# Optimization experiments

Measured on AMD Instinct MI355X. Metric: run time of the kernel, lower is better.

The kernel has to match this reference:

```python
import jax, jax.numpy as jnp
import numpy as np

NEG_INF = -9e15  # matches torch code's -9000000000000000.0
ALPHA = 0.1      # LeakyReLU negative slope


def setup_inputs() -> dict:
    key = jax.random.key(0)
    k1, k2, k3, k4 = jax.random.split(key, 4)
    N, D = 4096, 2048
    input_features = jax.random.normal(k1, (N, D), dtype=jnp.float32)
    adj_mat = jax.random.normal(k2, (N, N), dtype=jnp.float32)
    # parameters of GraphAttentionLayer(2048, 2048)
    W = jax.random.normal(k3, (D, D), dtype=jnp.float32) * 0.02
    a = jax.random.normal(k4, (2 * D, 1), dtype=jnp.float32) * 0.02
    return {"input_features": input_features, "adj_mat": adj_mat, "W": W, "a": a}


def reference(input_features, adj_mat, W, a):
    x = input_features  # [N, D]
    D = W.shape[1]
    # --- GNN.forward: cosine similarity adjacency ---
    dot = x @ x.T                                  # [N, N]
    lens = jnp.sqrt(jnp.sum(x * x, axis=1))        # [N]
    cos_sim = dot / (lens[:, None] * lens[None, :])
    new_adj = adj_mat * cos_sim                    # [N, N]
    # --- GraphAttentionLayer.forward ---
    h = x @ W                                      # [N, D]
    # concat trick: e_ij = leakyrelu(a1.h_i + a2.h_j), avoiding O(N^2*2D) tensor
    a1, a2 = a[:D, 0], a[D:, 0]
    s1 = h @ a1                                    # [N]
    s2 = h @ a2                                    # [N]
    e = jax.nn.leaky_relu(s1[:, None] + s2[None, :], ALPHA)  # [N, N]
    att_logits = jnp.where(new_adj > 0, e, NEG_INF)
    attention = jax.nn.softmax(att_logits, axis=1)  # dropout is identity at eval
    h_prime = attention @ h                        # [N, D]
    return jax.nn.elu(h_prime)                     # concat=True -> elu
```

## Files before the change

### kernel.cpp

```cpp
#include <hip/hip_runtime.h>
#include <hip/hip_bf16.h>
#include <cmath>

typedef unsigned short u16;
typedef unsigned char u8;
typedef unsigned int u32;
typedef __attribute__((ext_vector_type(8))) _Float16 f16x8;
typedef __attribute__((ext_vector_type(4))) float f32x4;

__device__ __forceinline__ float bf2f(u16 v) {
    union { u32 u; float f; } c; c.u = (u32)v << 16; return c.f;
}
__device__ __forceinline__ u16 f2bf(float f) {
    union { float f; u32 u; } c; c.f = f;
    u32 u = c.u;
    u += 0x7FFF + ((u >> 16) & 1);
    return (u16)(u >> 16);
}
__device__ __forceinline__ u16 f2h(float f) {
    _Float16 h = (_Float16)f; u16 r; __builtin_memcpy(&r, &h, 2); return r;
}
__device__ __forceinline__ float h2f(u16 b) {
    _Float16 h; __builtin_memcpy(&h, &b, 2); return (float)h;
}

__device__ __forceinline__ void gld_lds16(const void* g, void* l) {
    __builtin_amdgcn_global_load_lds(
        (const __attribute__((address_space(1))) void*)g,
        (__attribute__((address_space(3))) void*)l, 16, 0, 0);
}

__global__ __launch_bounds__(256) void sniff_kernel(const u16* __restrict__ x,
                                                    u32* __restrict__ flag) {
    const int t = threadIdx.x;
    int local = 0;
    for (int i = t; i < 4096; i += 256) {
        const int e = (x[i] >> 7) & 0xFF;
        if (e >= 110 && e <= 137) local++;
    }
#pragma unroll
    for (int o = 32; o > 0; o >>= 1) local += __shfl_down(local, o, 64);
    __shared__ int s[4];
    if ((t & 63) == 0) s[t >> 6] = local;
    __syncthreads();
    if (t == 0) {
        const int tot = s[0] + s[1] + s[2] + s[3];
        *flag = (tot >= 3200) ? 1u : 0u;
    }
}

__global__ __launch_bounds__(256) void prep_kernel(
    const void* __restrict__ xin, const void* __restrict__ Win,
    const void* __restrict__ ain,
    u16* __restrict__ xhi, u16* __restrict__ xlo,
    u16* __restrict__ WT, u16* __restrict__ aout,
    const u32* __restrict__ flag, int N, int D)
{
    __shared__ u16 tile[64][68];
    const bool isbf = (*flag != 0);
    const int b = blockIdx.x;
    const int t = threadIdx.x;

    if (b < 1024) {
        const long base = (long)b * 8192;
#pragma unroll
        for (int it = 0; it < 8; ++it) {
            const long i = base + (long)(it * 256 + t) * 4;
            float v[4];
            if (isbf) {
                ushort4 u = *(const ushort4*)((const u16*)xin + i);
                v[0] = bf2f(u.x); v[1] = bf2f(u.y); v[2] = bf2f(u.z); v[3] = bf2f(u.w);
            } else {
                float4 f = *(const float4*)((const float*)xin + i);
                v[0] = f.x; v[1] = f.y; v[2] = f.z; v[3] = f.w;
            }
            ushort4 hi, lo;
            u16* hp = &hi.x; u16* lp = &lo.x;
#pragma unroll
            for (int k = 0; k < 4; ++k) {
                _Float16 h = (_Float16)v[k];
                u16 hb; __builtin_memcpy(&hb, &h, 2);
                hp[k] = hb;
                lp[k] = f2h(v[k] - (float)h);
            }
            *(ushort4*)(xhi + i) = hi;
            *(ushort4*)(xlo + i) = lo;
        }
    } else if (b < 2048) {
        const int tt = b - 1024;
        const int bc = (tt & 31) * 64;
        const int br = (tt >> 5) * 64;
        const int lr = t >> 4;
        const int lc = (t & 15) * 4;
#pragma unroll
        for (int s = 0; s < 4; ++s) {
            const int r = lr + s * 16;
            float v[4];
            if (isbf) {
                ushort4 u = *(const ushort4*)((const u16*)Win + (size_t)(br + r) * D + bc + lc);
                v[0] = bf2f(u.x); v[1] = bf2f(u.y); v[2] = bf2f(u.z); v[3] = bf2f(u.w);
            } else {
                float4 f = *(const float4*)((const float*)Win + (size_t)(br + r) * D + bc + lc);
                v[0] = f.x; v[1] = f.y; v[2] = f.z; v[3] = f.w;
            }
            tile[r][lc + 0] = f2h(v[0]); tile[r][lc + 1] = f2h(v[1]);
            tile[r][lc + 2] = f2h(v[2]); tile[r][lc + 3] = f2h(v[3]);
        }
        __syncthreads();
#pragma unroll
        for (int s = 0; s < 4; ++s) {
            const int oc = lr + s * 16;
            ushort4 v;
            v.x = tile[lc + 0][oc]; v.y = tile[lc + 1][oc];
            v.z = tile[lc + 2][oc]; v.w = tile[lc + 3][oc];
            *(ushort4*)&WT[(size_t)(bc + oc) * D + br + lc] = v;
        }
    } else {
        for (int i = t; i < 2 * D; i += 256) {
            float v = isbf ? bf2f(((const u16*)ain)[i]) : ((const float*)ain)[i];
            aout[i] = f2h(v);
        }
    }
}

#define NMASK 528
#define MAXFIX 1024
__global__ __launch_bounds__(256, 2) void fused_mask_h(
    const u16* __restrict__ Xhi, const u16* __restrict__ Xlo, int ldx,
    u16* __restrict__ P, int N,
    const void* __restrict__ adj,
    const u16* __restrict__ WT, int D,
    u16* __restrict__ h,
    const u32* __restrict__ dflag)
{
    __shared__ alignas(16) u8 smem[32768];

    const int tid = threadIdx.x;
    const int wave = tid >> 6, lane = tid & 63;
    const int wr = wave >> 1, wc = wave & 1;
    const int srow = lane >> 2, slot = lane & 3;
    const int q = lane >> 4, mrow = lane & 15;

    if (blockIdx.x < NMASK) {
        const int idx = blockIdx.x;
        int bm = (int)((__builtin_sqrtf(8.0f * idx + 1.0f) - 1.0f) * 0.5f);
        while ((bm + 1) * (bm + 2) / 2 <= idx) ++bm;
        while (bm * (bm + 1) / 2 > idx) --bm;
        const int bn = idx - bm * (bm + 1) / 2;

        u16* smAh = (u16*)smem;
        u16* smBh = (u16*)(smem + 8192);

        const u16* Ah = Xhi + (size_t)bm * 128 * ldx;
        const u16* Bh = Xhi + (size_t)bn * 128 * ldx;

        f32x4 acc[4][4] = {};

        for (int kt = 0; kt < ldx; kt += 32) {
#pragma unroll
            for (int r = 0; r < 2; ++r) {
                const int rb = r * 64 + wave * 16;
                const size_t goff = (size_t)(rb + srow) * ldx + kt + slot * 8;
                gld_lds16(Ah + goff, &smAh[rb * 32]);
                gld_lds16(Bh + goff, &smBh[rb * 32]);
            }
            __syncthreads();

            f16x8 ah[4], bh[4];
#pragma unroll
            for (int i = 0; i < 4; ++i) {
                ah[i] = *(const f16x8*)&smAh[(wr * 64 + i * 16 + mrow) * 32 + q * 8];
                bh[i] = *(const f16x8*)&smBh[(wc * 64 + i * 16 + mrow) * 32 + q * 8];
            }
#pragma unroll
            for (int i = 0; i < 4; ++i)
#pragma unroll
                for (int j = 0; j < 4; ++j)
                    acc[i][j] = __builtin_amdgcn_mfma_f32_16x16x32_f16(
                        ah[i], bh[j], acc[i][j], 0, 0, 0);
            __syncthreads();
        }

        const bool isbf = (*dflag != 0);
        const u16* adjB = (const u16*)adj;
        const float* adjF = (const float*)adj;

        u8* sgn = smem;
        u32* list = (u32*)(smem + 24576);
        int* cntp = (int*)(smem + 28672);

        if (tid == 0) *cntp = 0;
        const float tau = isbf ? -1.0f : 0.125f;

#pragma unroll
        for (int i = 0; i < 4; ++i)
#pragma unroll
            for (int j = 0; j < 4; ++j)
#pragma unroll
                for (int r = 0; r < 4; ++r) {
                    const int rl = wr * 64 + i * 16 + q * 4 + r;
                    const int cl = wc * 64 + j * 16 + mrow;
                    const float v = acc[i][j][r];
                    sgn[rl * 132 + cl] = v > 0.f ? (u8)1
                                       : (v < 0.f ? (u8)2 : (u8)0);
                }
        __syncthreads();

#pragma unroll
        for (int i = 0; i < 4; ++i)
#pragma unroll
            for (int j = 0; j < 4; ++j)
#pragma unroll
                for (int r = 0; r < 4; ++r) {
                    const float v = acc[i][j][r];
                    if (__builtin_fabsf(v) < tau) {
                        const int rl = wr * 64 + i * 16 + q * 4 + r;
                        const int cl = wc * 64 + j * 16 + mrow;
                        const int ix = atomicAdd(cntp, 1);
                        if (ix < MAXFIX) list[ix] = (u32)((rl << 8) | cl);
                    }
                }
        __syncthreads();

        const int nfix = (*cntp < MAXFIX) ? *cntp : MAXFIX;
        for (int e = wave; e < nfix; e += 4) {
            const u32 pk = list[e];
            const int rl = (int)(pk >> 8), cl = (int)(pk & 255u);
            const u16* arh = Xhi + (size_t)(bm * 128 + rl) * ldx;
            const u16* arl = Xlo + (size_t)(bm * 128 + rl) * ldx;
            const u16* brh = Xhi + (size_t)(bn * 128 + cl) * ldx;
            const u16* brl = Xlo + (size_t)(bn * 128 + cl) * ldx;
            float ssum = 0.f;
#pragma unroll
            for (int kk = 0; kk < 4; ++kk) {
                const int k = kk * 512 + lane * 8;
                const f16x8 vah = *(const f16x8*)&arh[k];
                const f16x8 val2 = *(const f16x8*)&arl[k];
                const f16x8 vbh = *(const f16x8*)&brh[k];
                const f16x8 vbl = *(const f16x8*)&brl[k];
#pragma unroll
                for (int u = 0; u < 8; ++u)
                    ssum += ((float)vah[u] + (float)val2[u]) *
                            ((float)vbh[u] + (float)vbl[u]);
            }
#pragma unroll
            for (int o = 32; o > 0; o >>= 1) ssum += __shfl_xor(ssum, o, 64);
            if (lane == 0)
                sgn[rl * 132 + cl] = ssum > 0.f ? (u8)1
                                   : (ssum < 0.f ? (u8)2 : (u8)0);
        }
        __syncthreads();

        {
            const int c = tid & 127;
            const int r0 = tid >> 7;
#pragma unroll 4
            for (int s = 0; s < 64; ++s) {
                const int rr = r0 + 2 * s;
                const u8 s3 = sgn[rr * 132 + c];
                const size_t aidx = (size_t)(bm * 128 + rr) * N + bn * 128 + c;
                const float av = isbf ? bf2f(adjB[aidx]) : adjF[aidx];
                const bool f = (s3 == 1) ? (av > 0.f)
                             : (s3 == 2) ? (av < 0.f) : false;
                P[aidx] = f ? (u16)1 : (u16)0;
            }
        }

        if (bm != bn) {
            const int bl_ = tid & 63;
            const int a0 = tid >> 6;
#pragma unroll 4
            for (int s = 0; s < 32; ++s) {
                const int a = a0 + 4 * s;
#pragma unroll
                for (int hb = 0; hb < 2; ++hb) {
                    const int b = bl_ + 64 * hb;
                    const u8 s3 = sgn[b * 132 + a];
                    const size_t aidx = (size_t)(bn * 128 + a) * N + bm * 128 + b;
                    const float av = isbf ? bf2f(adjB[aidx]) : adjF[aidx];
                    const bool f = (s3 == 1) ? (av > 0.f)
                                 : (s3 == 2) ? (av < 0.f) : false;
                    P[aidx] = f ? (u16)1 : (u16)0;
                }
            }
        }
    } else {
        const int j = blockIdx.x - NMASK;
        const int bn = j & 15;
        const int bm = j >> 4;

        u16* smA = (u16*)smem;
        u16* smB = (u16*)(smem + 8192);

        const u16* Ab = Xhi + (size_t)bm * 128 * ldx;
        const u16* Bb = WT + (size_t)bn * 128 * D;

        f32x4 acc[4][4] = {};

        for (int kt = 0; kt < D; kt += 32) {
#pragma unroll
            for (int r = 0; r < 2; ++r) {
                const int rb = r * 64 + wave * 16;
                const int gr = rb + srow;
                gld_lds16(Ab + (size_t)gr * ldx + kt + slot * 8, &smA[rb * 32]);
                gld_lds16(Bb + (size_t)gr * D + kt + slot * 8, &smB[rb * 32]);
            }
            __syncthreads();

            f16x8 af[4], bfr[4];
#pragma unroll
            for (int i = 0; i < 4; ++i) {
                af[i]  = *(const f16x8*)&smA[(wr * 64 + i * 16 + mrow) * 32 + q * 8];
                bfr[i] = *(const f16x8*)&smB[(wc * 64 + i * 16 + mrow) * 32 + q * 8];
            }
#pragma unroll
            for (int i = 0; i < 4; ++i)
#pragma unroll
                for (int jj = 0; jj < 4; ++jj)
                    acc[i][jj] = __builtin_amdgcn_mfma_f32_16x16x32_f16(
                        af[i], bfr[jj], acc[i][jj], 0, 0, 0);
            __syncthreads();
        }

        const int col0 = bn * 128 + wc * 64 + mrow;
        const int row0 = bm * 128 + wr * 64 + q * 4;
#pragma unroll
        for (int i = 0; i < 4; ++i)
#pragma unroll
            for (int jj = 0; jj < 4; ++jj)
#pragma unroll
                for (int r = 0; r < 4; ++r)
                    h[(size_t)(row0 + i * 16 + r) * D + col0 + jj * 16] =
                        f2h(acc[i][jj][r]);
    }
}

__global__ __launch_bounds__(256) void post1_kernel(
    const u16* __restrict__ h, const u16* __restrict__ a,
    float* __restrict__ s1, float* __restrict__ s2,
    u16* __restrict__ hT, int N, int D)
{
    __shared__ u16 tile[64][68];
    __shared__ float r1[4], r2[4];
    const int b = blockIdx.x;
    const int t = threadIdx.x;

    if (b < N) {
        const u16* hr = h + (size_t)b * D;
        const int k0 = t * 8;
        float acc1 = 0.f, acc2 = 0.f;
#pragma unroll
        for (int u = 0; u < 8; u += 4) {
            ushort4 hv  = *(const ushort4*)&hr[k0 + u];
            ushort4 a1v = *(const ushort4*)&a[k0 + u];
            ushort4 a2v = *(const ushort4*)&a[D + k0 + u];
            acc1 += h2f(hv.x) * h2f(a1v.x) + h2f(hv.y) * h2f(a1v.y)
                  + h2f(hv.z) * h2f(a1v.z) + h2f(hv.w) * h2f(a1v.w);
            acc2 += h2f(hv.x) * h2f(a2v.x) + h2f(hv.y) * h2f(a2v.y)
                  + h2f(hv.z) * h2f(a2v.z) + h2f(hv.w) * h2f(a2v.w);
        }
        const int lane = t & 63, wv = t >> 6;
#pragma unroll
        for (int o = 32; o > 0; o >>= 1) {
            acc1 += __shfl_down(acc1, o, 64);
            acc2 += __shfl_down(acc2, o, 64);
        }
        if (lane == 0) { r1[wv] = acc1; r2[wv] = acc2; }
        __syncthreads();
        if (t == 0) {
            s1[b] = r1[0] + r1[1] + r1[2] + r1[3];
            s2[b] = r2[0] + r2[1] + r2[2] + r2[3];
        }
    } else {
        const int tt = b - N;
        const int bc = (tt & 31) * 64;
        const int br = (tt >> 5) * 64;
        const int lr = t >> 4;
        const int lc = (t & 15) * 4;
#pragma unroll
        for (int s = 0; s < 4; ++s) {
            const int r = lr + s * 16;
            ushort4 v = *(const ushort4*)&h[(size_t)(br + r) * D + bc + lc];
            tile[r][lc + 0] = v.x; tile[r][lc + 1] = v.y;
            tile[r][lc + 2] = v.z; tile[r][lc + 3] = v.w;
        }
        __syncthreads();
#pragma unroll
        for (int s = 0; s < 4; ++s) {
            const int oc = lr + s * 16;
            ushort4 v;
            v.x = tile[lc + 0][oc]; v.y = tile[lc + 1][oc];
            v.z = tile[lc + 2][oc]; v.w = tile[lc + 3][oc];
            *(ushort4*)&hT[(size_t)(bc + oc) * N + br + lc] = v;
        }
    }
}

__global__ __launch_bounds__(256) void softmax_kernel(
    u16* __restrict__ P, const float* __restrict__ s1,
    const float* __restrict__ s2, int N)
{
    const int row = blockIdx.x;
    const int t = threadIdx.x;
    const int lane = t & 63, wv = t >> 6;
    u16* prow = P + (size_t)row * N;
    const float s1v = s1[row];

    float e[16];
#pragma unroll
    for (int it = 0; it < 16; ++it) {
        const int j = it * 256 + t;
        const u16 f = prow[j];
        float ev = s1v + s2[j];
        ev = ev >= 0.f ? ev : 0.1f * ev;
        e[it] = f ? ev : -9.0e15f;
    }
    float m = -3.4e38f;
#pragma unroll
    for (int it = 0; it < 16; ++it) m = fmaxf(m, e[it]);
#pragma unroll
    for (int o = 32; o > 0; o >>= 1) m = fmaxf(m, __shfl_xor(m, o, 64));
    __shared__ float red[8];
    if (lane == 0) red[wv] = m;
    __syncthreads();
    m = fmaxf(fmaxf(red[0], red[1]), fmaxf(red[2], red[3]));

    float sum = 0.f;
#pragma unroll
    for (int it = 0; it < 16; ++it) {
        e[it] = expf(fminf(e[it] - m, 0.0f));
        sum += e[it];
    }
#pragma unroll
    for (int o = 32; o > 0; o >>= 1) sum += __shfl_xor(sum, o, 64);
    if (lane == 0) red[4 + wv] = sum;
    __syncthreads();
    sum = red[4] + red[5] + red[6] + red[7];
    const float inv = 1.f / fmaxf(sum, 1e-30f);
#pragma unroll
    for (int it = 0; it < 16; ++it) {
        const int j = it * 256 + t;
        prow[j] = f2h(e[it] * inv);
    }
}

__global__ __launch_bounds__(256, 2) void gemm_elu(
    const u16* __restrict__ A, int lda,
    const u16* __restrict__ B, int ldb,
    u16* __restrict__ C, int ldc,
    int K, const u32* __restrict__ dflag)
{
    __shared__ alignas(16) u16 smA[64 * 32];
    __shared__ alignas(16) u16 smB[128 * 32];

    const int tid = threadIdx.x;
    const int wave = tid >> 6, lane = tid & 63;
    const int bm = blockIdx.y, bn = blockIdx.x;

    const u16* Ab = A + (size_t)bm * 64 * lda;
    const u16* Bb = B + (size_t)bn * 128 * ldb;

    const int srow = lane >> 2, slot = lane & 3;
    const int q = lane >> 4, mrow = lane & 15;

    f32x4 acc[4][2] = {};

    for (int kt = 0; kt < K; kt += 32) {
        {
            const int rb = wave * 16;
            gld_lds16(Ab + (size_t)(rb + srow) * lda + kt + slot * 8, &smA[rb * 32]);
        }
#pragma unroll
        for (int r = 0; r < 2; ++r) {
            const int rb = r * 64 + wave * 16;
            gld_lds16(Bb + (size_t)(rb + srow) * ldb + kt + slot * 8, &smB[rb * 32]);
        }
        __syncthreads();

        f16x8 af[4], bfr[2];
#pragma unroll
        for (int i = 0; i < 4; ++i)
            af[i] = *(const f16x8*)&smA[(i * 16 + mrow) * 32 + q * 8];
#pragma unroll
        for (int j = 0; j < 2; ++j)
            bfr[j] = *(const f16x8*)&smB[(wave * 32 + j * 16 + mrow) * 32 + q * 8];
#pragma unroll
        for (int i = 0; i < 4; ++i)
#pragma unroll
            for (int j = 0; j < 2; ++j)
                acc[i][j] = __builtin_amdgcn_mfma_f32_16x16x32_f16(
                    af[i], bfr[j], acc[i][j], 0, 0, 0);
        __syncthreads();
    }

    const bool isbf = (*dflag != 0);
    float* outF = (float*)C;
    const int col0 = bn * 128 + wave * 32 + mrow;
    const int row0 = bm * 64 + q * 4;
#pragma unroll
    for (int i = 0; i < 4; ++i)
#pragma unroll
        for (int j = 0; j < 2; ++j)
#pragma unroll
            for (int r = 0; r < 4; ++r) {
                const int row = row0 + i * 16 + r;
                const int col = col0 + j * 16;
                const float v = acc[i][j][r];
                const float o = v > 0.0f ? v : expm1f(v);
                if (isbf) C[(size_t)row * ldc + col] = f2bf(o);
                else      outF[(size_t)row * ldc + col] = o;
            }
}

extern "C" void kernel_launch(void* const* d_in, const int* in_sizes, int n_in,
                              void* d_out, int out_size, void* d_ws, size_t ws_size,
                              hipStream_t stream)
{
    const void* x   = d_in[0];
    const void* adj = d_in[1];
    const void* W   = d_in[2];
    const void* a   = d_in[3];

    const int N = 4096, D = 2048;

    u16* xhi = (u16*)d_ws;
    u16* xlo = xhi + (size_t)N * D;
    u16* WT  = xlo + (size_t)N * D;
    u16* h   = WT  + (size_t)D * D;
    u16* P   = h   + (size_t)N * D;
    u16* af  = P   + (size_t)N * N;
    float* s1 = (float*)(af + 4096);
    float* s2 = s1 + N;
    u32* flag = (u32*)(s2 + N);

    sniff_kernel<<<1, 256, 0, stream>>>((const u16*)x, flag);
    prep_kernel<<<dim3(2049), 256, 0, stream>>>(x, W, a, xhi, xlo, WT, af,
                                                flag, N, D);
    fused_mask_h<<<dim3(NMASK + 512), 256, 0, stream>>>(
        xhi, xlo, D, P, N, adj, WT, D, h, flag);
    post1_kernel<<<dim3(N + 2048), 256, 0, stream>>>(h, af, s1, s2, xlo, N, D);
    softmax_kernel<<<dim3(N), 256, 0, stream>>>(P, s1, s2, N);
    gemm_elu<<<dim3(D / 128, N / 64), 256, 0, stream>>>(
        P, N, xlo, N, (u16*)d_out, D, N, flag);
}
```

Baseline: 469.4 us.

## Split mask and h GEMMs, use 256-row tiles with LDS double buffering

Splits the fused mask/h kernel into two kernels. The mask kernel now computes the full 256x256 X·Xᵀ tile grid instead of the symmetric lower triangle, and the h and final attention GEMMs move to 512-thread blocks with 256x128 tiles. All three GEMMs add double-buffered LDS staging and a block-index swizzle, aiming for better data reuse and overlap of loads with MFMA work. The mask kernel drops the symmetry trick, so it does about twice the X·Xᵀ FLOPs, and it writes P straight from registers with strided stores instead of going through an LDS sign buffer.

```diff
diff --git a/kernel.cpp b/kernel.cpp
--- a/kernel.cpp
+++ b/kernel.cpp
@@ -123,17 +123,137 @@
     }
 }
 
-#define NMASK 528
 #define MAXFIX 1024
-__global__ __launch_bounds__(256, 2) void fused_mask_h(
+#define MTAU 0.125f
+__global__ __launch_bounds__(512, 2) void mask_kernel(
     const u16* __restrict__ Xhi, const u16* __restrict__ Xlo, int ldx,
     u16* __restrict__ P, int N,
     const void* __restrict__ adj,
+    const u32* __restrict__ dflag)
+{
+    __shared__ alignas(16) u16 sm[2][2][256 * 32];
+
+    const int tid = threadIdx.x;
+    const int wave = tid >> 6, lane = tid & 63;
+    const int wr = wave >> 2, wc = wave & 3;
+    const int srow = lane >> 2, slot = lane & 3;
+    const int q = lane >> 4, mrow = lane & 15;
+
+    const int bid = blockIdx.x;
+    const int swz = (bid & 7) * 32 + (bid >> 3);
+    const int bm = swz >> 4, bn = swz & 15;
+
+    const u16* Ab = Xhi + (size_t)bm * 256 * ldx;
+    const u16* Bb = Xhi + (size_t)bn * 256 * ldx;
+
+    f32x4 acc[8][4] = {};
+
+    auto stage = [&](int buf, int kt) {
+#pragma unroll
+        for (int r = 0; r < 2; ++r) {
+            const int rb = r * 128 + wave * 16;
+            const size_t goff = (size_t)(rb + srow) * ldx + kt + slot * 8;
+            gld_lds16(Ab + goff, &sm[buf][0][rb * 32]);
+            gld_lds16(Bb + goff, &sm[buf][1][rb * 32]);
+        }
+    };
+
+    const int T = ldx >> 5;
+    stage(0, 0);
+    __syncthreads();
+    for (int t = 0; t < T; ++t) {
+        if (t + 1 < T) stage((t + 1) & 1, (t + 1) * 32);
+        const int buf = t & 1;
+        f16x8 a[8], b[4];
+#pragma unroll
+        for (int i = 0; i < 8; ++i)
+            a[i] = *(const f16x8*)&sm[buf][0][(wr * 128 + i * 16 + mrow) * 32 + q * 8];
+#pragma unroll
+        for (int j = 0; j < 4; ++j)
+            b[j] = *(const f16x8*)&sm[buf][1][(wc * 64 + j * 16 + mrow) * 32 + q * 8];
+#pragma unroll
+        for (int i = 0; i < 8; ++i)
+#pragma unroll
+            for (int j = 0; j < 4; ++j)
+                acc[i][j] = __builtin_amdgcn_mfma_f32_16x16x32_f16(
+                    a[i], b[j], acc[i][j], 0, 0, 0);
+        __syncthreads();
+    }
+
+    const bool isbf = (*dflag != 0);
+    const u16* adjB = (const u16*)adj;
+    const float* adjF = (const float*)adj;
+    const float tau = isbf ? -1.0f : MTAU;
+
+    u32* list = (u32*)&sm[0][0][0];
+    int* cntp = (int*)&sm[1][0][0];
+    if (tid == 0) *cntp = 0;
+    __syncthreads();
+
+#pragma unroll
+    for (int i = 0; i < 8; ++i)
+#pragma unroll
+        for (int j = 0; j < 4; ++j)
+#pragma unroll
+            for (int r = 0; r < 4; ++r)
+                if (__builtin_fabsf(acc[i][j][r]) < tau) {
+                    const int rl = wr * 128 + i * 16 + q * 4 + r;
+                    const int cl = wc * 64 + j * 16 + mrow;
+                    const int ix = atomicAdd(cntp, 1);
+                    if (ix < MAXFIX) list[ix] = (u32)((rl << 8) | cl);
+                }
+
+    const int row0 = bm * 256 + wr * 128 + q * 4;
+    const int col0 = bn * 256 + wc * 64 + mrow;
+#pragma unroll
+    for (int i = 0; i < 8; ++i)
+#pragma unroll
+        for (int j = 0; j < 4; ++j)
+#pragma unroll
+            for (int r = 0; r < 4; ++r) {
+                const int row = row0 + i * 16 + r;
+                const int col = col0 + j * 16;
+                const size_t aidx = (size_t)row * N + col;
+                const float av = isbf ? bf2f(adjB[aidx]) : adjF[aidx];
+                P[aidx] = (av * acc[i][j][r] > 0.0f) ? (u16)1 : (u16)0;
+            }
+    __syncthreads();
+
+    const int nfix = (*cntp < MAXFIX) ? *cntp : MAXFIX;
+    for (int e = wave; e < nfix; e += 8) {
+        const u32 pk = list[e];
+        const int rl = (int)(pk >> 8), cl = (int)(pk & 255u);
+        const u16* arh = Xhi + (size_t)(bm * 256 + rl) * ldx;
+        const u16* arl = Xlo + (size_t)(bm * 256 + rl) * ldx;
+        const u16* brh = Xhi + (size_t)(bn * 256 + cl) * ldx;
+        const u16* brl = Xlo + (size_t)(bn * 256 + cl) * ldx;
+        float ssum = 0.f;
+        for (int k = lane * 8; k < ldx; k += 512) {
+            const f16x8 vah = *(const f16x8*)&arh[k];
+            const f16x8 val2 = *(const f16x8*)&arl[k];
+            const f16x8 vbh = *(const f16x8*)&brh[k];
+            const f16x8 vbl = *(const f16x8*)&brl[k];
+#pragma unroll
+            for (int u = 0; u < 8; ++u)
+                ssum += ((float)vah[u] + (float)val2[u]) *
+                        ((float)vbh[u] + (float)vbl[u]);
+        }
+#pragma unroll
+        for (int o = 32; o > 0; o >>= 1) ssum += __shfl_xor(ssum, o, 64);
+        if (lane == 0) {
+            const size_t aidx = (size_t)(bm * 256 + rl) * N + bn * 256 + cl;
+            const float av = isbf ? bf2f(adjB[aidx]) : adjF[aidx];
+            P[aidx] = (av * ssum > 0.0f) ? (u16)1 : (u16)0;
+        }
+    }
+}
+
+__global__ __launch_bounds__(512, 2) void h_kernel(
+    const u16* __restrict__ Xhi, int ldx,
     const u16* __restrict__ WT, int D,
-    u16* __restrict__ h,
-    const u32* __restrict__ dflag)
-{
-    __shared__ alignas(16) u8 smem[32768];
+    u16* __restrict__ h)
+{
+    __shared__ alignas(16) u16 sm[2][256 * 32 + 128 * 32];
 
     const int tid = threadIdx.x;
     const int wave = tid >> 6, lane = tid & 63;
@@ -141,198 +261,59 @@
     const int srow = lane >> 2, slot = lane & 3;
     const int q = lane >> 4, mrow = lane & 15;
 
-    if (blockIdx.x < NMASK) {
-        const int idx = blockIdx.x;
-        int bm = (int)((__builtin_sqrtf(8.0f * idx + 1.0f) - 1.0f) * 0.5f);
-        while ((bm + 1) * (bm + 2) / 2 <= idx) ++bm;
-        while (bm * (bm + 1) / 2 > idx) --bm;
-        const int bn = idx - bm * (bm + 1) / 2;
-
-        u16* smAh = (u16*)smem;
-        u16* smBh = (u16*)(smem + 8192);
-
-        const u16* Ah = Xhi + (size_t)bm * 128 * ldx;
-        const u16* Bh = Xhi + (size_t)bn * 128 * ldx;
-
-        f32x4 acc[4][4] = {};
-
-        for (int kt = 0; kt < ldx; kt += 32) {
-#pragma unroll
-            for (int r = 0; r < 2; ++r) {
-                const int rb = r * 64 + wave * 16;
-                const size_t goff = (size_t)(rb + srow) * ldx + kt + slot * 8;
-                gld_lds16(Ah + goff, &smAh[rb * 32]);
-                gld_lds16(Bh + goff, &smBh[rb * 32]);
-            }
-            __syncthreads();
-
-            f16x8 ah[4], bh[4];
-#pragma unroll
-            for (int i = 0; i < 4; ++i) {
-                ah[i] = *(const f16x8*)&smAh[(wr * 64 + i * 16 + mrow) * 32 + q * 8];
-                bh[i] = *(const f16x8*)&smBh[(wc * 64 + i * 16 + mrow) * 32 + q * 8];
-            }
-#pragma unroll
-            for (int i = 0; i < 4; ++i)
-#pragma unroll
-                for (int j = 0; j < 4; ++j)
-                    acc[i][j] = __builtin_amdgcn_mfma_f32_16x16x32_f16(
-                        ah[i], bh[j], acc[i][j], 0, 0, 0);
-            __syncthreads();
-        }
-
-        const bool isbf = (*dflag != 0);
-        const u16* adjB = (const u16*)adj;
-        const float* adjF = (const float*)adj;
-
-        u8* sgn = smem;
-        u32* list = (u32*)(smem + 24576);
-        int* cntp = (int*)(smem + 28672);
-
-        if (tid == 0) *cntp = 0;
-        const float tau = isbf ? -1.0f : 0.125f;
-
+    const int bid = blockIdx.x;
+    const int swz = (bid & 7) * 32 + (bid >> 3);
+    const int bm = swz >> 4, bn = swz & 15;
+
+    const u16* Ab = Xhi + (size_t)bm * 256 * ldx;
+    const u16* Bb = WT + (size_t)bn * 128 * D;
+
+    f32x4 acc[4][4] = {};
+
+    auto stage = [&](int buf, int kt) {
+#pragma unroll
+        for (int r = 0; r < 2; ++r) {
+            const int rb = r * 128 + wave * 16;
+            gld_lds16(Ab + (size_t)(rb + srow) * ldx + kt + slot * 8,
+                      &sm[buf][rb * 32]);
+        }
+        const int rb = wave * 16;
+        gld_lds16(Bb + (size_t)(rb + srow) * D + kt + slot * 8,
+                  &sm[buf][256 * 32 + rb * 32]);
+    };
+
+    const int T = D >> 5;
+    stage(0, 0);
+    __syncthreads();
+    for (int t = 0; t < T; ++t) {
+        if (t + 1 < T) stage((t + 1) & 1, (t + 1) * 32);
+        const int buf = t & 1;
+        f16x8 a[4], b[4];
 #pragma unroll
         for (int i = 0; i < 4; ++i)
+            a[i] = *(const f16x8*)&sm[buf][(wr * 64 + i * 16 + mrow) * 32 + q * 8];
+#pragma unroll
+        for (int j = 0; j < 4; ++j)
+            b[j] = *(const f16x8*)&sm[buf][256 * 32 + (wc * 64 + j * 16 + mrow) * 32 + q * 8];
+#pragma unroll
+        for (int i = 0; i < 4; ++i)
 #pragma unroll
             for (int j = 0; j < 4; ++j)
-#pragma unroll
-                for (int r = 0; r < 4; ++r) {
-                    const int rl = wr * 64 + i * 16 + q * 4 + r;
-                    const int cl = wc * 64 + j * 16 + mrow;
-                    const float v = acc[i][j][r];
-                    sgn[rl * 132 + cl] = v > 0.f ? (u8)1
-                                       : (v < 0.f ? (u8)2 : (u8)0);
-                }
+                acc[i][j] = __builtin_amdgcn_mfma_f32_16x16x32_f16(
+                    a[i], b[j], acc[i][j], 0, 0, 0);
         __syncthreads();
-
-#pragma unroll
-        for (int i = 0; i < 4; ++i)
-#pragma unroll
-            for (int j = 0; j < 4; ++j)
-#pragma unroll
-                for (int r = 0; r < 4; ++r) {
-                    const float v = acc[i][j][r];
-                    if (__builtin_fabsf(v) < tau) {
-                        const int rl = wr * 64 + i * 16 + q * 4 + r;
-                        const int cl = wc * 64 + j * 16 + mrow;
-                        const int ix = atomicAdd(cntp, 1);
-                        if (ix < MAXFIX) list[ix] = (u32)((rl << 8) | cl);
-                    }
-                }
-        __syncthreads();
-
-        const int nfix = (*cntp < MAXFIX) ? *cntp : MAXFIX;
-        for (int e = wave; e < nfix; e += 4) {
-            const u32 pk = list[e];
-            const int rl = (int)(pk >> 8), cl = (int)(pk & 255u);
-            const u16* arh = Xhi + (size_t)(bm * 128 + rl) * ldx;
-            const u16* arl = Xlo + (size_t)(bm * 128 + rl) * ldx;
-            const u16* brh = Xhi + (size_t)(bn * 128 + cl) * ldx;
-            const u16* brl = Xlo + (size_t)(bn * 128 + cl) * ldx;
-            float ssum = 0.f;
-#pragma unroll
-            for (int kk = 0; kk < 4; ++kk) {
-                const int k = kk * 512 + lane * 8;
-                const f16x8 vah = *(const f16x8*)&arh[k];
-                const f16x8 val2 = *(const f16x8*)&arl[k];
-                const f16x8 vbh = *(const f16x8*)&brh[k];
-                const f16x8 vbl = *(const f16x8*)&brl[k];
-#pragma unroll
-                for (int u = 0; u < 8; ++u)
-                    ssum += ((float)vah[u] + (float)val2[u]) *
-                            ((float)vbh[u] + (float)vbl[u]);
-            }
-#pragma unroll
-            for (int o = 32; o > 0; o >>= 1) ssum += __shfl_xor(ssum, o, 64);
-            if (lane == 0)
-                sgn[rl * 132 + cl] = ssum > 0.f ? (u8)1
-                                   : (ssum < 0.f ? (u8)2 : (u8)0);
-        }
-        __syncthreads();
-
-        {
-            const int c = tid & 127;
-            const int r0 = tid >> 7;
-#pragma unroll 4
-            for (int s = 0; s < 64; ++s) {
-                const int rr = r0 + 2 * s;
-                const u8 s3 = sgn[rr * 132 + c];
-                const size_t aidx = (size_t)(bm * 128 + rr) * N + bn * 128 + c;
-                const float av = isbf ? bf2f(adjB[aidx]) : adjF[aidx];
-                const bool f = (s3 == 1) ? (av > 0.f)
-                             : (s3 == 2) ? (av < 0.f) : false;
-                P[aidx] = f ? (u16)1 : (u16)0;
-            }
-        }
-
-        if (bm != bn) {
-            const int bl_ = tid & 63;
-            const int a0 = tid >> 6;
-#pragma unroll 4
-            for (int s = 0; s < 32; ++s) {
-                const int a = a0 + 4 * s;
-#pragma unroll
-                for (int hb = 0; hb < 2; ++hb) {
-                    const int b = bl_ + 64 * hb;
-                    const u8 s3 = sgn[b * 132 + a];
-                    const size_t aidx = (size_t)(bn * 128 + a) * N + bm * 128 + b;
-                    const float av = isbf ? bf2f(adjB[aidx]) : adjF[aidx];
-                    const bool f = (s3 == 1) ? (av > 0.f)
-                                 : (s3 == 2) ? (av < 0.f) : false;
-                    P[aidx] = f ? (u16)1 : (u16)0;
-                }
-            }
-        }
-    } else {
-        const int j = blockIdx.x - NMASK;
-        const int bn = j & 15;
-        const int bm = j >> 4;
-
-        u16* smA = (u16*)smem;
-        u16* smB = (u16*)(smem + 8192);
-
-        const u16* Ab = Xhi + (size_t)bm * 128 * ldx;
-        const u16* Bb = WT + (size_t)bn * 128 * D;
-
-        f32x4 acc[4][4] = {};
-
-        for (int kt = 0; kt < D; kt += 32) {
-#pragma unroll
-            for (int r = 0; r < 2; ++r) {
-                const int rb = r * 64 + wave * 16;
-                const int gr = rb + srow;
-                gld_lds16(Ab + (size_t)gr * ldx + kt + slot * 8, &smA[rb * 32]);
-                gld_lds16(Bb + (size_t)gr * D + kt + slot * 8, &smB[rb * 32]);
-            }
-            __syncthreads();
-
-            f16x8 af[4], bfr[4];
-#pragma unroll
-            for (int i = 0; i < 4; ++i) {
-                af[i]  = *(const f16x8*)&smA[(wr * 64 + i * 16 + mrow) * 32 + q * 8];
-                bfr[i] = *(const f16x8*)&smB[(wc * 64 + i * 16 + mrow) * 32 + q * 8];
-            }
-#pragma unroll
-            for (int i = 0; i < 4; ++i)
-#pragma unroll
-                for (int jj = 0; jj < 4; ++jj)
-                    acc[i][jj] = __builtin_amdgcn_mfma_f32_16x16x32_f16(
-                        af[i], bfr[jj], acc[i][jj], 0, 0, 0);
-            __syncthreads();
-        }
-
-        const int col0 = bn * 128 + wc * 64 + mrow;
-        const int row0 = bm * 128 + wr * 64 + q * 4;
-#pragma unroll
-        for (int i = 0; i < 4; ++i)
-#pragma unroll
-            for (int jj = 0; jj < 4; ++jj)
-#pragma unroll
-                for (int r = 0; r < 4; ++r)
-                    h[(size_t)(row0 + i * 16 + r) * D + col0 + jj * 16] =
-                        f2h(acc[i][jj][r]);
-    }
+    }
+
+    const int row0 = bm * 256 + wr * 64 + q * 4;
+    const int col0 = bn * 128 + wc * 64 + mrow;
+#pragma unroll
+    for (int i = 0; i < 4; ++i)
+#pragma unroll
+        for (int j = 0; j < 4; ++j)
+#pragma unroll
+            for (int r = 0; r < 4; ++r)
+                h[(size_t)(row0 + i * 16 + r) * D + col0 + j * 16] =
+                    f2h(acc[i][j][r]);
 }
 
 __global__ __launch_bounds__(256) void post1_kernel(
@@ -444,63 +425,71 @@
     }
 }
 
-__global__ __launch_bounds__(256, 2) void gemm_elu(
+__global__ __launch_bounds__(512, 2) void gemm_elu(
     const u16* __restrict__ A, int lda,
     const u16* __restrict__ B, int ldb,
     u16* __restrict__ C, int ldc,
     int K, const u32* __restrict__ dflag)
 {
-    __shared__ alignas(16) u16 smA[64 * 32];
-    __shared__ alignas(16) u16 smB[128 * 32];
+    __shared__ alignas(16) u16 sm[2][256 * 32 + 128 * 32];
 
     const int tid = threadIdx.x;
     const int wave = tid >> 6, lane = tid & 63;
-    const int bm = blockIdx.y, bn = blockIdx.x;
-
-    const u16* Ab = A + (size_t)bm * 64 * lda;
-    const u16* Bb = B + (size_t)bn * 128 * ldb;
-
+    const int wr = wave >> 1, wc = wave & 1;
     const int srow = lane >> 2, slot = lane & 3;
     const int q = lane >> 4, mrow = lane & 15;
 
-    f32x4 acc[4][2] = {};
-
-    for (int kt = 0; kt < K; kt += 32) {
-        {
-            const int rb = wave * 16;
-            gld_lds16(Ab + (size_t)(rb + srow) * lda + kt + slot * 8, &smA[rb * 32]);
-        }
+    const int bid = blockIdx.x;
+    const int swz = (bid & 7) * 32 + (bid >> 3);
+    const int bm = swz >> 4, bn = swz & 15;
+
+    const u16* Ab = A + (size_t)bm * 256 * lda;
+    const u16* Bb = B + (size_t)bn * 128 * ldb;
+
+    f32x4 acc[4][4] = {};
+
+    auto stage = [&](int buf, int kt) {
 #pragma unroll
         for (int r = 0; r < 2; ++r) {
-            const int rb = r * 64 + wave * 16;
-            gld_lds16(Bb + (size_t)(rb + srow) * ldb + kt + slot * 8, &smB[rb * 32]);
-        }
-        __syncthreads();
-
-        f16x8 af[4], bfr[2];
+            const int rb = r * 128 + wave * 16;
+            gld_lds16(Ab + (size_t)(rb + srow) * lda + kt + slot * 8,
+                      &sm[buf][rb * 32]);
+        }
+        const int rb = wave * 16;
+        gld_lds16(Bb + (size_t)(rb + srow) * ldb + kt + slot * 8,
+                  &sm[buf][256 * 32 + rb * 32]);
+    };
+
+    const int T = K >> 5;
+    stage(0, 0);
+    __syncthreads();
+    for (int t = 0; t < T; ++t) {
+        if (t + 1 < T) stage((t + 1) & 1, (t + 1) * 32);
+        const int buf = t & 1;
+        f16x8 a[4], b[4];
 #pragma unroll
         for (int i = 0; i < 4; ++i)
-            af[i] = *(const f16x8*)&smA[(i * 16 + mrow) * 32 + q * 8];
-#pragma unroll
-        for (int j = 0; j < 2; ++j)
-            bfr[j] = *(const f16x8*)&smB[(wave * 32 + j * 16 + mrow) * 32 + q * 8];
+            a[i] = *(const f16x8*)&sm[buf][(wr * 64 + i * 16 + mrow) * 32 + q * 8];
+#pragma unroll
+        for (int j = 0; j < 4; ++j)
+            b[j] = *(const f16x8*)&sm[buf][256 * 32 + (wc * 64 + j * 16 + mrow) * 32 + q * 8];
 #pragma unroll
         for (int i = 0; i < 4; ++i)
 #pragma unroll
-            for (int j = 0; j < 2; ++j)
+            for (int j = 0; j < 4; ++j)
                 acc[i][j] = __builtin_amdgcn_mfma_f32_16x16x32_f16(
-                    af[i], bfr[j], acc[i][j], 0, 0, 0);
+                    a[i], b[j], acc[i][j], 0, 0, 0);
         __syncthreads();
     }
 
     const bool isbf = (*dflag != 0);
     float* outF = (float*)C;
-    const int col0 = bn * 128 + wave * 32 + mrow;
-    const int row0 = bm * 64 + q * 4;
+    const int row0 = bm * 256 + wr * 64 + q * 4;
+    const int col0 = bn * 128 + wc * 64 + mrow;
 #pragma unroll
     for (int i = 0; i < 4; ++i)
 #pragma unroll
-        for (int j = 0; j < 2; ++j)
+        for (int j = 0; j < 4; ++j)
 #pragma unroll
             for (int r = 0; r < 4; ++r) {
                 const int row = row0 + i * 16 + r;
@@ -536,10 +525,10 @@
     sniff_kernel<<<1, 256, 0, stream>>>((const u16*)x, flag);
     prep_kernel<<<dim3(2049), 256, 0, stream>>>(x, W, a, xhi, xlo, WT, af,
                                                 flag, N, D);
-    fused_mask_h<<<dim3(NMASK + 512), 256, 0, stream>>>(
-        xhi, xlo, D, P, N, adj, WT, D, h, flag);
+    mask_kernel<<<dim3(256), 512, 0, stream>>>(xhi, xlo, D, P, N, adj, flag);
+    h_kernel<<<dim3(256), 512, 0, stream>>>(xhi, D, WT, D, h);
     post1_kernel<<<dim3(N + 2048), 256, 0, stream>>>(h, af, s1, s2, xlo, N, D);
     softmax_kernel<<<dim3(N), 256, 0, stream>>>(P, s1, s2, N);
-    gemm_elu<<<dim3(D / 128, N / 64), 256, 0, stream>>>(
+    gemm_elu<<<dim3(256), 512, 0, stream>>>(
         P, N, xlo, N, (u16*)d_out, D, N, flag);
 }
```

After: 502.2 us. +7.0%, slower.

## Double-buffer GEMM mainloops with BK=64, XOR-swizzled LDS, and block swizzling

Applied to the files above, without the earlier changes.

Rewrites the mainloops of the fused mask/h GEMM and the attention·h GEMM to use double-buffered LDS with a K-step of 64, prefetching the next tile while MFMAs run on the current one. LDS rows are XOR-swizzled to avoid bank conflicts. The final GEMM grows from 64x128 to 128x128 tiles. Both launches use a 1-D grid remapped so that neighbouring blocks share operand rows, which should help L2 reuse. The aim is fewer barriers per K element and better latency hiding, at the cost of 64KB of LDS per block, which may reduce occupancy.

```diff
diff --git a/kernel.cpp b/kernel.cpp
--- a/kernel.cpp
+++ b/kernel.cpp
@@ -125,6 +125,7 @@
 
 #define NMASK 528
 #define MAXFIX 1024
+#define MTAU 0.125f
 __global__ __launch_bounds__(256, 2) void fused_mask_h(
     const u16* __restrict__ Xhi, const u16* __restrict__ Xlo, int ldx,
     u16* __restrict__ P, int N,
@@ -133,65 +134,83 @@
     u16* __restrict__ h,
     const u32* __restrict__ dflag)
 {
-    __shared__ alignas(16) u8 smem[32768];
+    __shared__ alignas(16) u16 sm[2][2][128 * 64];
 
     const int tid = threadIdx.x;
     const int wave = tid >> 6, lane = tid & 63;
     const int wr = wave >> 1, wc = wave & 1;
-    const int srow = lane >> 2, slot = lane & 3;
     const int q = lane >> 4, mrow = lane & 15;
-
-    if (blockIdx.x < NMASK) {
-        const int idx = blockIdx.x;
+    const int srow8 = lane >> 3;
+    const int gslot = (lane & 7) ^ srow8;
+
+    const int bid = blockIdx.x;
+    const int swz = (bid & 7) * 130 + (bid >> 3);
+
+    const bool isbf = (*dflag != 0);
+
+    if (swz < NMASK) {
+        const int idx = swz;
         int bm = (int)((__builtin_sqrtf(8.0f * idx + 1.0f) - 1.0f) * 0.5f);
         while ((bm + 1) * (bm + 2) / 2 <= idx) ++bm;
         while (bm * (bm + 1) / 2 > idx) --bm;
         const int bn = idx - bm * (bm + 1) / 2;
 
-        u16* smAh = (u16*)smem;
-        u16* smBh = (u16*)(smem + 8192);
-
-        const u16* Ah = Xhi + (size_t)bm * 128 * ldx;
-        const u16* Bh = Xhi + (size_t)bn * 128 * ldx;
+        const u16* Ab = Xhi + (size_t)bm * 128 * ldx;
+        const u16* Bb = Xhi + (size_t)bn * 128 * ldx;
 
         f32x4 acc[4][4] = {};
 
-        for (int kt = 0; kt < ldx; kt += 32) {
-#pragma unroll
-            for (int r = 0; r < 2; ++r) {
-                const int rb = r * 64 + wave * 16;
-                const size_t goff = (size_t)(rb + srow) * ldx + kt + slot * 8;
-                gld_lds16(Ah + goff, &smAh[rb * 32]);
-                gld_lds16(Bh + goff, &smBh[rb * 32]);
-            }
+#define STAGE_M(buf, kt)                                                     \
+        {                                                                    \
+            _Pragma("unroll")                                                \
+            for (int it = 0; it < 4; ++it) {                                 \
+                const int c = wave * 4 + it;                                 \
+                const int row = c * 8 + srow8;                               \
+                const size_t go = (size_t)row * ldx + (kt) + gslot * 8;      \
+                gld_lds16(Ab + go, &sm[buf][0][c * 512]);                    \
+                gld_lds16(Bb + go, &sm[buf][1][c * 512]);                    \
+            }                                                                \
+        }
+
+        const int T = ldx >> 6;
+        STAGE_M(0, 0);
+        __syncthreads();
+        for (int t = 0; t < T; ++t) {
+            if (t + 1 < T) STAGE_M((t + 1) & 1, (t + 1) * 64);
+            const int buf = t & 1;
+            f16x8 a[2][4], b[2][4];
+#pragma unroll
+            for (int ks = 0; ks < 2; ++ks)
+#pragma unroll
+                for (int i = 0; i < 4; ++i) {
+                    const int ra = wr * 64 + i * 16 + mrow;
+                    const int rb = wc * 64 + i * 16 + mrow;
+                    const int sa = ((q + 4 * ks) ^ (mrow & 7)) * 8;
+                    a[ks][i] = *(const f16x8*)&sm[buf][0][ra * 64 + sa];
+                    b[ks][i] = *(const f16x8*)&sm[buf][1][rb * 64 + sa];
+                }
+#pragma unroll
+            for (int i = 0; i < 4; ++i)
+#pragma unroll
+                for (int j = 0; j < 4; ++j) {
+                    acc[i][j] = __builtin_amdgcn_mfma_f32_16x16x32_f16(
+                        a[0][i], b[0][j], acc[i][j], 0, 0, 0);
+                    acc[i][j] = __builtin_amdgcn_mfma_f32_16x16x32_f16(
+                        a[1][i], b[1][j], acc[i][j], 0, 0, 0);
+                }
             __syncthreads();
-
-            f16x8 ah[4], bh[4];
-#pragma unroll
-            for (int i = 0; i < 4; ++i) {
-                ah[i] = *(const f16x8*)&smAh[(wr * 64 + i * 16 + mrow) * 32 + q * 8];
-                bh[i] = *(const f16x8*)&smBh[(wc * 64 + i * 16 + mrow) * 32 + q * 8];
-            }
-#pragma unroll
-            for (int i = 0; i < 4; ++i)
-#pragma unroll
-                for (int j = 0; j < 4; ++j)
-                    acc[i][j] = __builtin_amdgcn_mfma_f32_16x16x32_f16(
-                        ah[i], bh[j], acc[i][j], 0, 0, 0);
-            __syncthreads();
-        }
-
-        const bool isbf = (*dflag != 0);
+        }
+#undef STAGE_M
+
         const u16* adjB = (const u16*)adj;
         const float* adjF = (const float*)adj;
-
-        u8* sgn = smem;
-        u32* list = (u32*)(smem + 24576);
-        int* cntp = (int*)(smem + 28672);
+        const float tau = isbf ? -1.0f : MTAU;
+
+        u8* sgn = (u8*)sm;
+        u32* list = (u32*)((u8*)sm + 24576);
+        int* cntp = (int*)((u8*)sm + 28672);
 
         if (tid == 0) *cntp = 0;
-        const float tau = isbf ? -1.0f : 0.125f;
-
 #pragma unroll
         for (int i = 0; i < 4; ++i)
 #pragma unroll
@@ -211,15 +230,13 @@
 #pragma unroll
             for (int j = 0; j < 4; ++j)
 #pragma unroll
-                for (int r = 0; r < 4; ++r) {
-                    const float v = acc[i][j][r];
-                    if (__builtin_fabsf(v) < tau) {
+                for (int r = 0; r < 4; ++r)
+                    if (__builtin_fabsf(acc[i][j][r]) < tau) {
                         const int rl = wr * 64 + i * 16 + q * 4 + r;
                         const int cl = wc * 64 + j * 16 + mrow;
                         const int ix = atomicAdd(cntp, 1);
                         if (ix < MAXFIX) list[ix] = (u32)((rl << 8) | cl);
                     }
-                }
         __syncthreads();
 
         const int nfix = (*cntp < MAXFIX) ? *cntp : MAXFIX;
@@ -285,45 +302,60 @@
             }
         }
     } else {
-        const int j = blockIdx.x - NMASK;
+        const int j = swz - NMASK;
         const int bn = j & 15;
         const int bm = j >> 4;
 
-        u16* smA = (u16*)smem;
-        u16* smB = (u16*)(smem + 8192);
-
         const u16* Ab = Xhi + (size_t)bm * 128 * ldx;
         const u16* Bb = WT + (size_t)bn * 128 * D;
 
         f32x4 acc[4][4] = {};
 
-        for (int kt = 0; kt < D; kt += 32) {
-#pragma unroll
-            for (int r = 0; r < 2; ++r) {
-                const int rb = r * 64 + wave * 16;
-                const int gr = rb + srow;
-                gld_lds16(Ab + (size_t)gr * ldx + kt + slot * 8, &smA[rb * 32]);
-                gld_lds16(Bb + (size_t)gr * D + kt + slot * 8, &smB[rb * 32]);
-            }
+#define STAGE_H(buf, kt)                                                     \
+        {                                                                    \
+            _Pragma("unroll")                                                \
+            for (int it = 0; it < 4; ++it) {                                 \
+                const int c = wave * 4 + it;                                 \
+                const int row = c * 8 + srow8;                               \
+                gld_lds16(Ab + (size_t)row * ldx + (kt) + gslot * 8,         \
+                          &sm[buf][0][c * 512]);                             \
+                gld_lds16(Bb + (size_t)row * D + (kt) + gslot * 8,           \
+                          &sm[buf][1][c * 512]);                             \
+            }                                                                \
+        }
+
+        const int T = D >> 6;
+        STAGE_H(0, 0);
+        __syncthreads();
+        for (int t = 0; t < T; ++t) {
+            if (t + 1 < T) STAGE_H((t + 1) & 1, (t + 1) * 64);
+            const int buf = t & 1;
+            f16x8 a[2][4], b[2][4];
+#pragma unroll
+            for (int ks = 0; ks < 2; ++ks)
+#pragma unroll
+                for (int i = 0; i < 4; ++i) {
+                    const int ra = wr * 64 + i * 16 + mrow;
+                    const int rb = wc * 64 + i * 16 + mrow;
+                    const int sa = ((q + 4 * ks) ^ (mrow & 7)) * 8;
+                    a[ks][i] = *(const f16x8*)&sm[buf][0][ra * 64 + sa];
+                    b[ks][i] = *(const f16x8*)&sm[buf][1][rb * 64 + sa];
+                }
+#pragma unroll
+            for (int i = 0; i < 4; ++i)
+#pragma unroll
+                for (int jj = 0; jj < 4; ++jj) {
+                    acc[i][jj] = __builtin_amdgcn_mfma_f32_16x16x32_f16(
+                        a[0][i], b[0][jj], acc[i][jj], 0, 0, 0);
+                    acc[i][jj] = __builtin_amdgcn_mfma_f32_16x16x32_f16(
+                        a[1][i], b[1][jj], acc[i][jj], 0, 0, 0);
+                }
             __syncthreads();
-
-            f16x8 af[4], bfr[4];
-#pragma unroll
-            for (int i = 0; i < 4; ++i) {
-                af[i]  = *(const f16x8*)&smA[(wr * 64 + i * 16 + mrow) * 32 + q * 8];
-                bfr[i] = *(const f16x8*)&smB[(wc * 64 + i * 16 + mrow) * 32 + q * 8];
-            }
-#pragma unroll
-            for (int i = 0; i < 4; ++i)
-#pragma unroll
-                for (int jj = 0; jj < 4; ++jj)
-                    acc[i][jj] = __builtin_amdgcn_mfma_f32_16x16x32_f16(
-                        af[i], bfr[jj], acc[i][jj], 0, 0, 0);
-            __syncthreads();
-        }
-
+        }
+#undef STAGE_H
+
+        const int row0 = bm * 128 + wr * 64 + q * 4;
         const int col0 = bn * 128 + wc * 64 + mrow;
-        const int row0 = bm * 128 + wr * 64 + q * 4;
 #pragma unroll
         for (int i = 0; i < 4; ++i)
 #pragma unroll
@@ -450,57 +482,76 @@
     u16* __restrict__ C, int ldc,
     int K, const u32* __restrict__ dflag)
 {
-    __shared__ alignas(16) u16 smA[64 * 32];
-    __shared__ alignas(16) u16 smB[128 * 32];
+    __shared__ alignas(16) u16 sm[2][2][128 * 64];
 
     const int tid = threadIdx.x;
     const int wave = tid >> 6, lane = tid & 63;
-    const int bm = blockIdx.y, bn = blockIdx.x;
-
-    const u16* Ab = A + (size_t)bm * 64 * lda;
+    const int wr = wave >> 1, wc = wave & 1;
+    const int q = lane >> 4, mrow = lane & 15;
+    const int srow8 = lane >> 3;
+    const int gslot = (lane & 7) ^ srow8;
+
+    const int bid = blockIdx.x;
+    const int swz = (bid & 7) * 64 + (bid >> 3);
+    const int bm = swz >> 4;
+    const int bn = swz & 15;
+
+    const u16* Ab = A + (size_t)bm * 128 * lda;
     const u16* Bb = B + (size_t)bn * 128 * ldb;
 
-    const int srow = lane >> 2, slot = lane & 3;
-    const int q = lane >> 4, mrow = lane & 15;
-
-    f32x4 acc[4][2] = {};
-
-    for (int kt = 0; kt < K; kt += 32) {
-        {
-            const int rb = wave * 16;
-            gld_lds16(Ab + (size_t)(rb + srow) * lda + kt + slot * 8, &smA[rb * 32]);
-        }
-#pragma unroll
-        for (int r = 0; r < 2; ++r) {
-            const int rb = r * 64 + wave * 16;
-            gld_lds16(Bb + (size_t)(rb + srow) * ldb + kt + slot * 8, &smB[rb * 32]);
-        }
-        __syncthreads();
-
-        f16x8 af[4], bfr[2];
+    f32x4 acc[4][4] = {};
+
+#define STAGE_E(buf, kt)                                                     \
+    {                                                                        \
+        _Pragma("unroll")                                                    \
+        for (int it = 0; it < 4; ++it) {                                     \
+            const int c = wave * 4 + it;                                     \
+            const int row = c * 8 + srow8;                                   \
+            gld_lds16(Ab + (size_t)row * lda + (kt) + gslot * 8,             \
+                      &sm[buf][0][c * 512]);                                 \
+            gld_lds16(Bb + (size_t)row * ldb + (kt) + gslot * 8,             \
+                      &sm[buf][1][c * 512]);                                 \
+        }                                                                    \
+    }
+
+    const int T = K >> 6;
+    STAGE_E(0, 0);
+    __syncthreads();
+    for (int t = 0; t < T; ++t) {
+        if (t + 1 < T) STAGE_E((t + 1) & 1, (t + 1) * 64);
+        const int buf = t & 1;
+        f16x8 a[2][4], b[2][4];
+#pragma unroll
+        for (int ks = 0; ks < 2; ++ks)
+#pragma unroll
+            for (int i = 0; i < 4; ++i) {
+                const int ra = wr * 64 + i * 16 + mrow;
+                const int rb = wc * 64 + i * 16 + mrow;
+                const int sa = ((q + 4 * ks) ^ (mrow & 7)) * 8;
+                a[ks][i] = *(const f16x8*)&sm[buf][0][ra * 64 + sa];
+                b[ks][i] = *(const f16x8*)&sm[buf][1][rb * 64 + sa];
+            }
 #pragma unroll
         for (int i = 0; i < 4; ++i)
-            af[i] = *(const f16x8*)&smA[(i * 16 + mrow) * 32 + q * 8];
-#pragma unroll
-        for (int j = 0; j < 2; ++j)
-            bfr[j] = *(const f16x8*)&smB[(wave * 32 + j * 16 + mrow) * 32 + q * 8];
-#pragma unroll
-        for (int i = 0; i < 4; ++i)
-#pragma unroll
-            for (int j = 0; j < 2; ++j)
+#pragma unroll
+            for (int j = 0; j < 4; ++j) {
                 acc[i][j] = __builtin_amdgcn_mfma_f32_16x16x32_f16(
-                    af[i], bfr[j], acc[i][j], 0, 0, 0);
-        __syncthreads();
-    }
+                    a[0][i], b[0][j], acc[i][j], 0, 0, 0);
+                acc[i][j] = __builtin_amdgcn_mfma_f32_16x16x32_f16(
+                    a[1][i], b[1][j], acc[i][j], 0, 0, 0);
+            }
+        __syncthreads();
+    }
+#undef STAGE_E
 
     const bool isbf = (*dflag != 0);
     float* outF = (float*)C;
-    const int col0 = bn * 128 + wave * 32 + mrow;
-    const int row0 = bm * 64 + q * 4;
+    const int row0 = bm * 128 + wr * 64 + q * 4;
+    const int col0 = bn * 128 + wc * 64 + mrow;
 #pragma unroll
     for (int i = 0; i < 4; ++i)
 #pragma unroll
-        for (int j = 0; j < 2; ++j)
+        for (int j = 0; j < 4; ++j)
 #pragma unroll
             for (int r = 0; r < 4; ++r) {
                 const int row = row0 + i * 16 + r;
@@ -536,10 +587,10 @@
     sniff_kernel<<<1, 256, 0, stream>>>((const u16*)x, flag);
     prep_kernel<<<dim3(2049), 256, 0, stream>>>(x, W, a, xhi, xlo, WT, af,
                                                 flag, N, D);
-    fused_mask_h<<<dim3(NMASK + 512), 256, 0, stream>>>(
+    fused_mask_h<<<dim3(1040), 256, 0, stream>>>(
         xhi, xlo, D, P, N, adj, WT, D, h, flag);
     post1_kernel<<<dim3(N + 2048), 256, 0, stream>>>(h, af, s1, s2, xlo, N, D);
     softmax_kernel<<<dim3(N), 256, 0, stream>>>(P, s1, s2, N);
-    gemm_elu<<<dim3(D / 128, N / 64), 256, 0, stream>>>(
+    gemm_elu<<<dim3(512), 256, 0, stream>>>(
         P, N, xlo, N, (u16*)d_out, D, N, flag);
 }
```

Result: slower. 552.1 us (+17.6%).
